# Optimization experiments

Measured on AMD Instinct MI355X. Metric: run time of the kernel, lower is better.

Reference implementation:

```python
import jax, jax.numpy as jnp
import numpy as np

FMAP = 64
SIGMA = 0.5
FRAC = 0.9
N_MESH = 162  # ~vertices of level-2 icosphere (10*4^2+2)
B, C = 32, 512


def _build_weight(key):
    # Surrogate for Icosahedron(level).halfmesh_locs: N 2-D locations in [-1,1]^2.
    locs = jax.random.uniform(key, (N_MESH, 2), minval=-1.0, maxval=1.0)
    px = 0.5 * FMAP * FRAC * locs[:, 0] + FMAP / 2  # [N]
    py = 0.5 * FMAP * FRAC * locs[:, 1] + FMAP / 2  # [N]
    grid = jnp.arange(FMAP, dtype=jnp.float32) + 0.5
    gridx, gridy = jnp.meshgrid(grid, grid, indexing='ij')  # [H,W]
    scale = 1.0 / np.sqrt(2 * np.pi * SIGMA ** 2)
    d2 = (gridx[:, :, None] - px) ** 2 + (gridy[:, :, None] - py) ** 2  # [H,W,N]
    w = scale * jnp.exp(-d2 / (2 * SIGMA ** 2))
    w = w / w.sum((0, 1), keepdims=True)  # normalize per mesh point
    return w.astype(jnp.float32)


def setup_inputs() -> dict:
    key = jax.random.key(0)
    kx, kw = jax.random.split(key)
    x = jax.random.normal(kx, (B, C, FMAP, FMAP), dtype=jnp.float32)
    weight = _build_weight(kw)  # [H, W, N]
    return {"x": x, "weight": weight}


def reference(x, weight):
    # Original: (x.unsqueeze(-1) * weight[None,None]).sum((2,3)).transpose(1,2)
    # i.e. a grid-to-mesh GEMM: [B,C,H,W] x [H,W,N] -> [B,N,C]
    return jnp.einsum('bchw,hwn->bnc', x, weight)
```

## Files before the change

### kernel.cpp

```cpp
#include <hip/hip_runtime.h>
#include <cstdint>

constexpr int KDIM = 4096;
constexpr int NDIM = 162;
constexpr int NPAD = 176;
constexpr int NT   = 11;
constexpr int CDIM = 512;
constexpr int BM   = 64;
constexpr int BK   = 128;
constexpr int NCHUNK = KDIM / BK;
constexpr int WBYTES = 4 * NT * 64 * 16;
constexpr int TOTAL_PACK = KDIM * NPAD;
constexpr int TSTRIDE = 177;

typedef float f32x4 __attribute__((ext_vector_type(4)));
typedef short s16x8 __attribute__((ext_vector_type(8)));

__device__ __forceinline__ ushort f2bf(float f) {
  uint32_t u = __builtin_bit_cast(uint32_t, f);
  u += 0x7FFFu + ((u >> 16) & 1u);
  return (ushort)(u >> 16);
}

__device__ __forceinline__ void gll16(const void* g, void* l) {
  __builtin_amdgcn_global_load_lds(
      (const __attribute__((address_space(1))) uint32_t*)(uintptr_t)g,
      (__attribute__((address_space(3))) uint32_t*)(uintptr_t)l,
      16, 0, 0);
}

__global__ void pack_w_kernel(const float* __restrict__ w, ushort* __restrict__ wp) {
  int idx = blockIdx.x * 512 + threadIdx.x;
  int e    = idx & 7;
  int lane = (idx >> 3) & 63;
  int t3   = idx >> 9;
  int tn   = t3 % NT;
  int kst  = t3 / NT;
  int k = kst * 32 + (lane >> 4) * 8 + e;
  int n = tn * 16 + (lane & 15);
  float v = (n < NDIM) ? w[k * NDIM + n] : 0.0f;
  wp[idx] = f2bf(v);
}

__device__ __forceinline__ void stage_chunk(const ushort* wp, char* smem_c,
                                            int buf, int kc, int wid, int lane) {
  const char* gbase = (const char*)wp + (size_t)kc * WBYTES;
  char* lbase = smem_c + buf * WBYTES;
#pragma unroll
  for (int r = 0; r < 6; ++r) {
    int rr = r * 8 + wid;
    if (rr < 44) gll16(gbase + rr * 1024 + (size_t)lane * 16, lbase + rr * 1024);
  }
}

__global__ __launch_bounds__(512, 2) void fmap_gemm(
    const float* __restrict__ x, const ushort* __restrict__ wp,
    float* __restrict__ out) {
  __shared__ char smem[2 * WBYTES];
  const int tid  = threadIdx.x;
  const int lane = tid & 63;
  const int wid  = tid >> 6;
  const int wm   = wid & 3;
  const int kh   = wid >> 2;

  const int m0  = blockIdx.x * BM;
  const int row = m0 + wm * 16 + (lane & 15);
  const int g   = lane >> 4;
  const int ks0 = kh * 2;

  const float* xrow = x + (size_t)row * KDIM + g * 8;

  f32x4 acc[NT];
#pragma unroll
  for (int t = 0; t < NT; ++t) acc[t] = f32x4{0.f, 0.f, 0.f, 0.f};

  stage_chunk(wp, smem, 0, 0, wid, lane);
  float4 a_c[4];
  {
    const float* pb = xrow + ks0 * 32;
    a_c[0] = ((const float4*)pb)[0];
    a_c[1] = ((const float4*)pb)[1];
    a_c[2] = ((const float4*)(pb + 32))[0];
    a_c[3] = ((const float4*)(pb + 32))[1];
  }

  for (int kc = 0; kc < NCHUNK; ++kc) {
    const int cur = kc & 1, nxt = cur ^ 1;
    const bool has_next = (kc + 1 < NCHUNK);

    if (has_next) {
      stage_chunk(wp, smem, nxt, kc + 1, wid, lane);
      if (wid < 4) asm volatile("s_waitcnt vmcnt(6)" ::: "memory");
      else         asm volatile("s_waitcnt vmcnt(5)" ::: "memory");
    } else {
      asm volatile("s_waitcnt vmcnt(0)" ::: "memory");
    }
    __syncthreads();

    float4 a_n[4];
    if (has_next) {
      const float* pb = xrow + (kc + 1) * BK + ks0 * 32;
      a_n[0] = ((const float4*)pb)[0];
      a_n[1] = ((const float4*)pb)[1];
      a_n[2] = ((const float4*)(pb + 32))[0];
      a_n[3] = ((const float4*)(pb + 32))[1];
    }

    s16x8 af0, af1;
    af0[0] = (short)f2bf(a_c[0].x); af0[1] = (short)f2bf(a_c[0].y);
    af0[2] = (short)f2bf(a_c[0].z); af0[3] = (short)f2bf(a_c[0].w);
    af0[4] = (short)f2bf(a_c[1].x); af0[5] = (short)f2bf(a_c[1].y);
    af0[6] = (short)f2bf(a_c[1].z); af0[7] = (short)f2bf(a_c[1].w);
    af1[0] = (short)f2bf(a_c[2].x); af1[1] = (short)f2bf(a_c[2].y);
    af1[2] = (short)f2bf(a_c[2].z); af1[3] = (short)f2bf(a_c[2].w);
    af1[4] = (short)f2bf(a_c[3].x); af1[5] = (short)f2bf(a_c[3].y);
    af1[6] = (short)f2bf(a_c[3].z); af1[7] = (short)f2bf(a_c[3].w);

    const char* bb = smem + cur * WBYTES + (size_t)lane * 16;
#pragma unroll
    for (int t = 0; t < NT; ++t) {
      s16x8 b0 = *(const s16x8*)(bb + (size_t)((ks0 * NT + t) * 64) * 16);
      s16x8 b1 = *(const s16x8*)(bb + (size_t)(((ks0 + 1) * NT + t) * 64) * 16);
      acc[t] = __builtin_amdgcn_mfma_f32_16x16x32_bf16(af0, b0, acc[t], 0, 0, 0);
      acc[t] = __builtin_amdgcn_mfma_f32_16x16x32_bf16(af1, b1, acc[t], 0, 0, 0);
    }
    __syncthreads();

#pragma unroll
    for (int q = 0; q < 4; ++q) a_c[q] = a_n[q];
  }

  float* tile = (float*)smem;
  const int ncol  = lane & 15;
  const int rbase = wm * 16 + g * 4;
  if (kh == 0) {
#pragma unroll
    for (int t = 0; t < NT; ++t)
#pragma unroll
      for (int j = 0; j < 4; ++j)
        tile[(rbase + j) * TSTRIDE + t * 16 + ncol] = acc[t][j];
  }
  __syncthreads();
  if (kh == 1) {
#pragma unroll
    for (int t = 0; t < NT; ++t)
#pragma unroll
      for (int j = 0; j < 4; ++j)
        tile[(rbase + j) * TSTRIDE + t * 16 + ncol] += acc[t][j];
  }
  __syncthreads();

  const int bidx = m0 >> 9;
  const int c0   = m0 & 511;
  float* obase = out + (size_t)bidx * (NDIM * CDIM) + c0;
#pragma unroll
  for (int r = 0; r < 6; ++r) {
    int idx = r * 512 + tid;
    if (idx < NDIM * 16) {
      int n  = idx >> 4;
      int cq = idx & 15;
      float4 v;
      v.x = tile[(cq * 4 + 0) * TSTRIDE + n];
      v.y = tile[(cq * 4 + 1) * TSTRIDE + n];
      v.z = tile[(cq * 4 + 2) * TSTRIDE + n];
      v.w = tile[(cq * 4 + 3) * TSTRIDE + n];
      *(float4*)(obase + n * CDIM + cq * 4) = v;
    }
  }
}

extern "C" void kernel_launch(void* const* d_in, const int* in_sizes, int n_in,
                              void* d_out, int out_size, void* d_ws, size_t ws_size,
                              hipStream_t stream) {
  const float* x = (const float*)d_in[0];
  const float* w = (const float*)d_in[1];
  float* outp    = (float*)d_out;
  ushort* wp     = (ushort*)d_ws;

  pack_w_kernel<<<TOTAL_PACK / 512, 512, 0, stream>>>(w, wp);
  fmap_gemm<<<(32 * CDIM) / BM, 512, 0, stream>>>(x, wp, outp);
}
```

Baseline: 406.7 us.

## Halve K-chunk to cut LDS footprint and raise occupancy to four blocks

Halves the K chunk staged per iteration from 128 to 64. Each wave-half now runs one 32-wide MFMA step instead of two, which halves the LDS weight buffers and the per-thread A-register footprint. Launch bounds now ask for four blocks per CU instead of two, aiming to hide memory latency through occupancy rather than deeper per-block work. The explicit vmcnt waits are removed, so the code relies on the barrier to order the asynchronous LDS loads. That risks a race, and the doubled iteration count adds barrier overhead. The 64-VGPR budget at that occupancy may also force register spills.

```diff
diff --git a/kernel.cpp b/kernel.cpp
--- a/kernel.cpp
+++ b/kernel.cpp
@@ -7,11 +7,12 @@
 constexpr int NT   = 11;
 constexpr int CDIM = 512;
 constexpr int BM   = 64;
-constexpr int BK   = 128;
+constexpr int BK   = 64;
 constexpr int NCHUNK = KDIM / BK;
-constexpr int WBYTES = 4 * NT * 64 * 16;
+constexpr int WBYTES = 2 * NT * 64 * 16;
 constexpr int TOTAL_PACK = KDIM * NPAD;
 constexpr int TSTRIDE = 177;
+constexpr int SMEM_BYTES = 64 * TSTRIDE * 4;
 
 typedef float f32x4 __attribute__((ext_vector_type(4)));
 typedef short s16x8 __attribute__((ext_vector_type(8)));
@@ -47,16 +48,16 @@
   const char* gbase = (const char*)wp + (size_t)kc * WBYTES;
   char* lbase = smem_c + buf * WBYTES;
 #pragma unroll
-  for (int r = 0; r < 6; ++r) {
+  for (int r = 0; r < 3; ++r) {
     int rr = r * 8 + wid;
-    if (rr < 44) gll16(gbase + rr * 1024 + (size_t)lane * 16, lbase + rr * 1024);
+    if (rr < 22) gll16(gbase + rr * 1024 + (size_t)lane * 16, lbase + rr * 1024);
   }
 }
 
-__global__ __launch_bounds__(512, 2) void fmap_gemm(
+__global__ __launch_bounds__(512, 4) void fmap_gemm(
     const float* __restrict__ x, const ushort* __restrict__ wp,
     float* __restrict__ out) {
-  __shared__ char smem[2 * WBYTES];
+  __shared__ char smem[SMEM_BYTES];
   const int tid  = threadIdx.x;
   const int lane = tid & 63;
   const int wid  = tid >> 6;
@@ -66,68 +67,46 @@
   const int m0  = blockIdx.x * BM;
   const int row = m0 + wm * 16 + (lane & 15);
   const int g   = lane >> 4;
-  const int ks0 = kh * 2;
 
-  const float* xrow = x + (size_t)row * KDIM + g * 8;
+  const float* xrow = x + (size_t)row * KDIM + g * 8 + kh * 32;
 
   f32x4 acc[NT];
 #pragma unroll
   for (int t = 0; t < NT; ++t) acc[t] = f32x4{0.f, 0.f, 0.f, 0.f};
 
   stage_chunk(wp, smem, 0, 0, wid, lane);
-  float4 a_c[4];
-  {
-    const float* pb = xrow + ks0 * 32;
-    a_c[0] = ((const float4*)pb)[0];
-    a_c[1] = ((const float4*)pb)[1];
-    a_c[2] = ((const float4*)(pb + 32))[0];
-    a_c[3] = ((const float4*)(pb + 32))[1];
-  }
+  float4 a_c0, a_c1;
+  a_c0 = ((const float4*)xrow)[0];
+  a_c1 = ((const float4*)xrow)[1];
+  __syncthreads();
 
   for (int kc = 0; kc < NCHUNK; ++kc) {
-    const int cur = kc & 1, nxt = cur ^ 1;
+    const int cur = kc & 1;
     const bool has_next = (kc + 1 < NCHUNK);
 
+    float4 a_n0, a_n1;
     if (has_next) {
-      stage_chunk(wp, smem, nxt, kc + 1, wid, lane);
-      if (wid < 4) asm volatile("s_waitcnt vmcnt(6)" ::: "memory");
-      else         asm volatile("s_waitcnt vmcnt(5)" ::: "memory");
-    } else {
-      asm volatile("s_waitcnt vmcnt(0)" ::: "memory");
-    }
-    __syncthreads();
-
-    float4 a_n[4];
-    if (has_next) {
-      const float* pb = xrow + (kc + 1) * BK + ks0 * 32;
-      a_n[0] = ((const float4*)pb)[0];
-      a_n[1] = ((const float4*)pb)[1];
-      a_n[2] = ((const float4*)(pb + 32))[0];
-      a_n[3] = ((const float4*)(pb + 32))[1];
+      stage_chunk(wp, smem, cur ^ 1, kc + 1, wid, lane);
+      const float* pb = xrow + (kc + 1) * BK;
+      a_n0 = ((const float4*)pb)[0];
+      a_n1 = ((const float4*)pb)[1];
     }
 
-    s16x8 af0, af1;
-    af0[0] = (short)f2bf(a_c[0].x); af0[1] = (short)f2bf(a_c[0].y);
-    af0[2] = (short)f2bf(a_c[0].z); af0[3] = (short)f2bf(a_c[0].w);
-    af0[4] = (short)f2bf(a_c[1].x); af0[5] = (short)f2bf(a_c[1].y);
-    af0[6] = (short)f2bf(a_c[1].z); af0[7] = (short)f2bf(a_c[1].w);
-    af1[0] = (short)f2bf(a_c[2].x); af1[1] = (short)f2bf(a_c[2].y);
-    af1[2] = (short)f2bf(a_c[2].z); af1[3] = (short)f2bf(a_c[2].w);
-    af1[4] = (short)f2bf(a_c[3].x); af1[5] = (short)f2bf(a_c[3].y);
-    af1[6] = (short)f2bf(a_c[3].z); af1[7] = (short)f2bf(a_c[3].w);
+    s16x8 af;
+    af[0] = (short)f2bf(a_c0.x); af[1] = (short)f2bf(a_c0.y);
+    af[2] = (short)f2bf(a_c0.z); af[3] = (short)f2bf(a_c0.w);
+    af[4] = (short)f2bf(a_c1.x); af[5] = (short)f2bf(a_c1.y);
+    af[6] = (short)f2bf(a_c1.z); af[7] = (short)f2bf(a_c1.w);
 
     const char* bb = smem + cur * WBYTES + (size_t)lane * 16;
 #pragma unroll
     for (int t = 0; t < NT; ++t) {
-      s16x8 b0 = *(const s16x8*)(bb + (size_t)((ks0 * NT + t) * 64) * 16);
-      s16x8 b1 = *(const s16x8*)(bb + (size_t)(((ks0 + 1) * NT + t) * 64) * 16);
-      acc[t] = __builtin_amdgcn_mfma_f32_16x16x32_bf16(af0, b0, acc[t], 0, 0, 0);
-      acc[t] = __builtin_amdgcn_mfma_f32_16x16x32_bf16(af1, b1, acc[t], 0, 0, 0);
+      s16x8 b0 = *(const s16x8*)(bb + (size_t)((kh * NT + t) * 64) * 16);
+      acc[t] = __builtin_amdgcn_mfma_f32_16x16x32_bf16(af, b0, acc[t], 0, 0, 0);
     }
+
     __syncthreads();
-
-#pragma unroll
-    for (int q = 0; q < 4; ++q) a_c[q] = a_n[q];
+    a_c0 = a_n0; a_c1 = a_n1;
   }
 
   float* tile = (float*)smem;
```

Result: faster. 396.4 us (-2.5%).
